# Kernel tuning notes

Hardware: AMD Instinct MI355X
Metric: run time of the kernel (lower is better)

Reference implementation:

```python
import jax, jax.numpy as jnp
import numpy as np

S, B_BOX, C = 7, 2, 20
LAMBDA_COORD = 5.0
LAMBDA_NOOBJ = 0.5


def _iou(b1, b2):
    # b1, b2: [..., 4] in (cx, cy, w, h) format
    area1 = b1[..., 2] * b1[..., 3]
    area2 = b2[..., 2] * b2[..., 3]
    max_left = jnp.maximum(b1[..., 0] - b1[..., 2] / 2, b2[..., 0] - b2[..., 2] / 2)
    min_right = jnp.minimum(b1[..., 0] + b1[..., 2] / 2, b2[..., 0] + b2[..., 2] / 2)
    max_top = jnp.maximum(b1[..., 1] - b1[..., 3] / 2, b2[..., 1] - b2[..., 3] / 2)
    min_bottom = jnp.minimum(b1[..., 1] + b1[..., 3] / 2, b2[..., 1] + b2[..., 3] / 2)
    iw = jnp.maximum(min_right - max_left, 0.0)
    ih = jnp.maximum(min_bottom - max_top, 0.0)
    inter = iw * ih
    union = area1 + area2 - inter
    return jnp.where(inter > 0.0, inter / union, 0.0)


def setup_inputs() -> dict:
    key = jax.random.key(0)
    k1, k2, k3 = jax.random.split(key, 3)
    batch = 16384
    shape = (batch, S, S, C + 5 * B_BOX)  # [..., 30]
    pred = jax.random.uniform(k1, shape, dtype=jnp.float32)
    target = jax.random.uniform(k2, shape, dtype=jnp.float32)
    # objectness flag must be exactly 1.0 to trigger the obj branch
    obj_flag = jax.random.bernoulli(k3, 0.3, shape[:-1]).astype(jnp.float32)
    target = target.at[..., 0].set(obj_flag)
    return {"pred": pred, "target": target}


def reference(pred, target):
    batch = pred.shape[0]
    pred = pred.reshape(-1, S, S, C + 5 * B_BOX)
    target = target.reshape(-1, S, S, C + 5 * B_BOX)

    obj = (target[..., 0] == 1.0)          # [b,S,S] bool
    obj_f = obj.astype(pred.dtype)
    noobj_f = 1.0 - obj_f

    gt = target[..., 1:5]
    box1 = pred[..., 1:5]                   # predictor 1 box
    box2 = target[..., 6:10]                # NOTE: original code uses target's 2nd box
    iou1 = jax.lax.stop_gradient(_iou(box1, gt))
    iou2 = jax.lax.stop_gradient(_iou(box2, gt))
    resp1 = iou1 > iou2                     # predictor 1 responsible (strict >)
    r1 = resp1[..., None]

    # coord losses (responsible predictor)
    pxy = jnp.where(r1, pred[..., 1:3], pred[..., 6:8])
    txy = jnp.where(r1, target[..., 1:3], target[..., 6:8])
    pwh = jnp.where(r1, pred[..., 3:5], pred[..., 8:10])
    twh = jnp.where(r1, target[..., 3:5], target[..., 8:10])
    cell_xy = jnp.sum((pxy - txy) ** 2, axis=-1)
    cell_wh = jnp.sum((jnp.sqrt(pwh) - jnp.sqrt(twh)) ** 2, axis=-1)

    # obj confidence loss: responsible conf vs its iou
    conf_resp = jnp.where(resp1, pred[..., 0], pred[..., 5])
    iou_resp = jnp.where(resp1, iou1, iou2)
    cell_obj = (conf_resp - iou_resp) ** 2

    # noobj: non-responsible conf in obj cells; both confs in empty cells
    conf_other = jnp.where(resp1, pred[..., 5], pred[..., 0])
    cell_noobj_obj = conf_other ** 2
    cell_noobj_empty = pred[..., 0] ** 2 + pred[..., 5] ** 2

    cell_class = jnp.sum((pred[..., 10:] - target[..., 10:]) ** 2, axis=-1)

    loss_coord_xy = LAMBDA_COORD * jnp.sum(obj_f * cell_xy)
    loss_coord_wh = LAMBDA_COORD * jnp.sum(obj_f * cell_wh)
    loss_obj = jnp.sum(obj_f * cell_obj)
    loss_noobj = LAMBDA_NOOBJ * (jnp.sum(obj_f * cell_noobj_obj) + jnp.sum(noobj_f * cell_noobj_empty))
    loss_class = jnp.sum(obj_f * cell_class)
    loss = loss_coord_xy + loss_coord_wh + loss_obj + loss_noobj + loss_class

    bs = jnp.asarray(batch, pred.dtype)
    return ((loss_coord_xy + loss_coord_wh) / bs,
            loss_obj / bs,
            loss_noobj / bs,
            loss_class / bs,
            loss / bs)
```

## Files before the change

### kernel.cpp

```cpp
#include <hip/hip_runtime.h>

#define NCH 30
#define F2PC 15
#define F4PC 1920
#define CPB 256
#define THREADS 256
#define GRID_BLOCKS 512

typedef float fvec2 __attribute__((ext_vector_type(2)));
typedef float fvec4 __attribute__((ext_vector_type(4)));

__device__ __forceinline__ float iou_fn(float x1, float y1, float w1, float h1,
                                        float x2, float y2, float w2, float h2) {
    float a1 = w1 * h1, a2 = w2 * h2;
    float left  = fmaxf(x1 - w1 * 0.5f, x2 - w2 * 0.5f);
    float right = fminf(x1 + w1 * 0.5f, x2 + w2 * 0.5f);
    float top   = fmaxf(y1 - h1 * 0.5f, y2 - h2 * 0.5f);
    float bot   = fminf(y1 + h1 * 0.5f, y2 + h2 * 0.5f);
    float iw = fmaxf(right - left, 0.0f);
    float ih = fmaxf(bot - top, 0.0f);
    float inter = iw * ih;
    float uni = a1 + a2 - inter;
    return (inter > 0.0f) ? (inter / uni) : 0.0f;
}

__device__ __forceinline__ void cell_losses(const float* p, const float* t,
                                            float& coord, float& lobj,
                                            float& lnoobj, float& lclass) {
    float obj_f = (t[0] == 1.0f) ? 1.0f : 0.0f;

    float iou1 = iou_fn(p[1], p[2], p[3], p[4], t[1], t[2], t[3], t[4]);
    float iou2 = iou_fn(t[6], t[7], t[8], t[9], t[1], t[2], t[3], t[4]);
    bool r = iou1 > iou2;

    float px = r ? p[1] : p[6], py = r ? p[2] : p[7];
    float pw = r ? p[3] : p[8], ph = r ? p[4] : p[9];
    float tx = r ? t[1] : t[6], ty = r ? t[2] : t[7];
    float tw = r ? t[3] : t[8], th = r ? t[4] : t[9];

    float dx = px - tx, dy = py - ty;
    float cxy = dx * dx + dy * dy;
    float swv = sqrtf(pw) - sqrtf(tw), shv = sqrtf(ph) - sqrtf(th);
    float cwh = swv * swv + shv * shv;

    float conf_resp  = r ? p[0] : p[5];
    float iou_resp   = r ? iou1 : iou2;
    float conf_other = r ? p[5] : p[0];
    float dconf = conf_resp - iou_resp;

    coord  += obj_f * (cxy + cwh);
    lobj   += obj_f * dconf * dconf;
    lnoobj += obj_f * conf_other * conf_other
            + (1.0f - obj_f) * (p[0] * p[0] + p[5] * p[5]);

    float cls = 0.0f;
#pragma unroll
    for (int i = 10; i < NCH; i++) { float e = p[i] - t[i]; cls += e * e; }
    lclass += obj_f * cls;
}

__global__ __launch_bounds__(THREADS) void yolo_main(
        const fvec4* __restrict__ pred4, const fvec4* __restrict__ targ4,
        float4* __restrict__ partials, int nchunks_full, int n_cells) {
    __shared__ fvec4 sp4[F4PC];
    __shared__ fvec4 st4[F4PC];

    const int tid = threadIdx.x;
    float coord = 0.f, lobj = 0.f, lnoobj = 0.f, lclass = 0.f;

    fvec4 rp[8], rt[8];
    const bool extra = tid < (F4PC - 7 * THREADS);

    int c = blockIdx.x;
    bool have = c < nchunks_full;
    if (have) {
        const long long b = (long long)c * F4PC;
#pragma unroll
        for (int k = 0; k < 7; k++) {
            rp[k] = __builtin_nontemporal_load(pred4 + b + tid + k * THREADS);
            rt[k] = __builtin_nontemporal_load(targ4 + b + tid + k * THREADS);
        }
        if (extra) {
            rp[7] = __builtin_nontemporal_load(pred4 + b + 7 * THREADS + tid);
            rt[7] = __builtin_nontemporal_load(targ4 + b + 7 * THREADS + tid);
        }
    }

    while (have) {
        int cn = c + gridDim.x;
        bool have_n = cn < nchunks_full;

        __syncthreads();
#pragma unroll
        for (int k = 0; k < 7; k++) {
            sp4[tid + k * THREADS] = rp[k];
            st4[tid + k * THREADS] = rt[k];
        }
        if (extra) {
            sp4[7 * THREADS + tid] = rp[7];
            st4[7 * THREADS + tid] = rt[7];
        }
        __syncthreads();

        if (have_n) {
            const long long b = (long long)cn * F4PC;
#pragma unroll
            for (int k = 0; k < 7; k++) {
                rp[k] = __builtin_nontemporal_load(pred4 + b + tid + k * THREADS);
                rt[k] = __builtin_nontemporal_load(targ4 + b + tid + k * THREADS);
            }
            if (extra) {
                rp[7] = __builtin_nontemporal_load(pred4 + b + 7 * THREADS + tid);
                rt[7] = __builtin_nontemporal_load(targ4 + b + 7 * THREADS + tid);
            }
        }

        {
            float p[NCH], t[NCH];
            const fvec2* pp = reinterpret_cast<const fvec2*>(sp4) + tid * F2PC;
            const fvec2* tp = reinterpret_cast<const fvec2*>(st4) + tid * F2PC;
#pragma unroll
            for (int k = 0; k < F2PC; k++) { fvec2 v = pp[k]; p[2 * k] = v.x; p[2 * k + 1] = v.y; }
#pragma unroll
            for (int k = 0; k < F2PC; k++) { fvec2 v = tp[k]; t[2 * k] = v.x; t[2 * k + 1] = v.y; }
            cell_losses(p, t, coord, lobj, lnoobj, lclass);
        }

        c = cn; have = have_n;
    }

    if (blockIdx.x == 0) {
        int cell = nchunks_full * CPB + tid;
        if (cell < n_cells) {
            float p[NCH], t[NCH];
            const fvec2* pp = reinterpret_cast<const fvec2*>(pred4) + (long long)cell * F2PC;
            const fvec2* tp = reinterpret_cast<const fvec2*>(targ4) + (long long)cell * F2PC;
#pragma unroll
            for (int k = 0; k < F2PC; k++) { fvec2 v = pp[k]; p[2 * k] = v.x; p[2 * k + 1] = v.y; }
#pragma unroll
            for (int k = 0; k < F2PC; k++) { fvec2 v = tp[k]; t[2 * k] = v.x; t[2 * k + 1] = v.y; }
            cell_losses(p, t, coord, lobj, lnoobj, lclass);
        }
    }

#pragma unroll
    for (int off = 32; off > 0; off >>= 1) {
        coord  += __shfl_down(coord, off);
        lobj   += __shfl_down(lobj, off);
        lnoobj += __shfl_down(lnoobj, off);
        lclass += __shfl_down(lclass, off);
    }

    __shared__ float red[4][4];
    int lane = tid & 63;
    int wid  = tid >> 6;
    if (lane == 0) {
        red[wid][0] = coord; red[wid][1] = lobj;
        red[wid][2] = lnoobj; red[wid][3] = lclass;
    }
    __syncthreads();
    if (tid == 0) {
        float s0 = 0.f, s1 = 0.f, s2 = 0.f, s3 = 0.f;
        for (int w = 0; w < 4; w++) {
            s0 += red[w][0]; s1 += red[w][1];
            s2 += red[w][2]; s3 += red[w][3];
        }
        partials[blockIdx.x] = make_float4(s0, s1, s2, s3);
    }
}

__global__ __launch_bounds__(THREADS) void yolo_reduce(
        const float4* __restrict__ partials, int nparts,
        float* __restrict__ out, double inv_bs) {
    double s0 = 0.0, s1 = 0.0, s2 = 0.0, s3 = 0.0;
    for (int i = threadIdx.x; i < nparts; i += THREADS) {
        float4 v = partials[i];
        s0 += (double)v.x; s1 += (double)v.y;
        s2 += (double)v.z; s3 += (double)v.w;
    }
#pragma unroll
    for (int off = 32; off > 0; off >>= 1) {
        s0 += __shfl_down(s0, off);
        s1 += __shfl_down(s1, off);
        s2 += __shfl_down(s2, off);
        s3 += __shfl_down(s3, off);
    }
    __shared__ double red[4][4];
    int lane = threadIdx.x & 63;
    int wid  = threadIdx.x >> 6;
    if (lane == 0) {
        red[wid][0] = s0; red[wid][1] = s1;
        red[wid][2] = s2; red[wid][3] = s3;
    }
    __syncthreads();
    if (threadIdx.x == 0) {
        double a0 = 0, a1 = 0, a2 = 0, a3 = 0;
        for (int w = 0; w < 4; w++) {
            a0 += red[w][0]; a1 += red[w][1];
            a2 += red[w][2]; a3 += red[w][3];
        }
        double cd = a0 * 5.0 * inv_bs;
        double o  = a1 * inv_bs;
        double n  = a2 * 0.5 * inv_bs;
        double cl = a3 * inv_bs;
        out[0] = (float)cd;
        out[1] = (float)o;
        out[2] = (float)n;
        out[3] = (float)cl;
        out[4] = (float)(cd + o + n + cl);
    }
}

extern "C" void kernel_launch(void* const* d_in, const int* in_sizes, int n_in,
                              void* d_out, int out_size, void* d_ws, size_t ws_size,
                              hipStream_t stream) {
    const fvec4* pred4 = (const fvec4*)d_in[0];
    const fvec4* targ4 = (const fvec4*)d_in[1];
    float* out = (float*)d_out;
    float4* partials = (float4*)d_ws;

    int n_cells = in_sizes[0] / NCH;
    int batch   = n_cells / 49;
    int nchunks_full = n_cells / CPB;

    int grid = (nchunks_full <= 0) ? 1
             : (nchunks_full < GRID_BLOCKS ? nchunks_full : GRID_BLOCKS);

    yolo_main<<<grid, THREADS, 0, stream>>>(pred4, targ4, partials, nchunks_full, n_cells);
    yolo_reduce<<<1, THREADS, 0, stream>>>(partials, grid, out, 1.0 / (double)batch);
}
```

Baseline: 188.4 us.

## Use atomic work-stealing counter for chunk scheduling and drop nontemporal loads

Replaces the static grid-stride chunk assignment with a global atomic counter, so blocks grab the next chunk dynamically and the tail imbalance from an uneven chunks-per-block split shrinks. The counter lives at the start of the workspace and is cleared with an added memset before each launch. The per-iteration barrier is moved to publish the fetched index through shared memory. Global loads also switch from nontemporal to plain cached loads. The trade-off is an extra memset launch plus one atomic per chunk. There is also a possible race: thread 0 can overwrite the shared index in the first loop iteration before every thread has read the initial value.

```diff
diff --git a/kernel.cpp b/kernel.cpp
--- a/kernel.cpp
+++ b/kernel.cpp
@@ -61,9 +61,11 @@
 
 __global__ __launch_bounds__(THREADS) void yolo_main(
         const fvec4* __restrict__ pred4, const fvec4* __restrict__ targ4,
-        float4* __restrict__ partials, int nchunks_full, int n_cells) {
+        int* __restrict__ ctr, float4* __restrict__ partials,
+        int nchunks_full, int n_cells) {
     __shared__ fvec4 sp4[F4PC];
     __shared__ fvec4 st4[F4PC];
+    __shared__ int s_next;
 
     const int tid = threadIdx.x;
     float coord = 0.f, lobj = 0.f, lnoobj = 0.f, lclass = 0.f;
@@ -71,26 +73,29 @@
     fvec4 rp[8], rt[8];
     const bool extra = tid < (F4PC - 7 * THREADS);
 
-    int c = blockIdx.x;
+    if (tid == 0) s_next = atomicAdd(ctr, 1);
+    __syncthreads();
+    int c = s_next;
     bool have = c < nchunks_full;
     if (have) {
         const long long b = (long long)c * F4PC;
 #pragma unroll
         for (int k = 0; k < 7; k++) {
-            rp[k] = __builtin_nontemporal_load(pred4 + b + tid + k * THREADS);
-            rt[k] = __builtin_nontemporal_load(targ4 + b + tid + k * THREADS);
+            rp[k] = pred4[b + tid + k * THREADS];
+            rt[k] = targ4[b + tid + k * THREADS];
         }
         if (extra) {
-            rp[7] = __builtin_nontemporal_load(pred4 + b + 7 * THREADS + tid);
-            rt[7] = __builtin_nontemporal_load(targ4 + b + 7 * THREADS + tid);
+            rp[7] = pred4[b + 7 * THREADS + tid];
+            rt[7] = targ4[b + 7 * THREADS + tid];
         }
     }
 
     while (have) {
-        int cn = c + gridDim.x;
+        if (tid == 0) s_next = atomicAdd(ctr, 1);
+
+        __syncthreads();
+        int cn = s_next;
         bool have_n = cn < nchunks_full;
-
-        __syncthreads();
 #pragma unroll
         for (int k = 0; k < 7; k++) {
             sp4[tid + k * THREADS] = rp[k];
@@ -106,12 +111,12 @@
             const long long b = (long long)cn * F4PC;
 #pragma unroll
             for (int k = 0; k < 7; k++) {
-                rp[k] = __builtin_nontemporal_load(pred4 + b + tid + k * THREADS);
-                rt[k] = __builtin_nontemporal_load(targ4 + b + tid + k * THREADS);
+                rp[k] = pred4[b + tid + k * THREADS];
+                rt[k] = targ4[b + tid + k * THREADS];
             }
             if (extra) {
-                rp[7] = __builtin_nontemporal_load(pred4 + b + 7 * THREADS + tid);
-                rt[7] = __builtin_nontemporal_load(targ4 + b + 7 * THREADS + tid);
+                rp[7] = pred4[b + 7 * THREADS + tid];
+                rt[7] = targ4[b + 7 * THREADS + tid];
             }
         }
 
@@ -217,7 +222,8 @@
     const fvec4* pred4 = (const fvec4*)d_in[0];
     const fvec4* targ4 = (const fvec4*)d_in[1];
     float* out = (float*)d_out;
-    float4* partials = (float4*)d_ws;
+    int*    ctr      = (int*)d_ws;
+    float4* partials = (float4*)d_ws + 1;
 
     int n_cells = in_sizes[0] / NCH;
     int batch   = n_cells / 49;
@@ -226,6 +232,7 @@
     int grid = (nchunks_full <= 0) ? 1
              : (nchunks_full < GRID_BLOCKS ? nchunks_full : GRID_BLOCKS);
 
-    yolo_main<<<grid, THREADS, 0, stream>>>(pred4, targ4, partials, nchunks_full, n_cells);
+    hipMemsetAsync(ctr, 0, 16, stream);
+    yolo_main<<<grid, THREADS, 0, stream>>>(pred4, targ4, ctr, partials, nchunks_full, n_cells);
     yolo_reduce<<<1, THREADS, 0, stream>>>(partials, grid, out, 1.0 / (double)batch);
 }
```

Result: slower. 209.3 us (+11.1%).
